# Performance work log

Measured on AMD Instinct MI355X. Metric: run time of the kernel, lower is better.

Reference implementation:

```python
import jax, jax.numpy as jnp
import numpy as np

EPS = 1e-8


def setup_inputs() -> dict:
    key = jax.random.key(0)
    ks = jax.random.split(key, 3)
    B, d_in, d_sae = 2048, 2048, 16384
    x = jax.random.normal(ks[0], (B, 2, d_in), dtype=jnp.float32)
    W_enc = jax.random.normal(ks[1], (d_in, d_sae), dtype=jnp.float32) / (d_in ** 0.5)
    W_dec = jax.random.normal(ks[2], (d_sae, d_in), dtype=jnp.float32) / (d_sae ** 0.5)
    b_enc = jnp.zeros((d_sae,), dtype=jnp.float32)
    b_dec = jnp.zeros((d_in,), dtype=jnp.float32)
    return {"x": x, "W_enc": W_enc, "W_dec": W_dec, "b_enc": b_enc,
            "b_dec": b_dec, "k": 64, "h": 8192}


def _encode(x, W_enc, b_enc, k):
    # x: (N, d_in) -> z: (N, d_sae), top-k sparsified with relu on kept values
    pre = x @ W_enc + b_enc
    v, i = jax.lax.top_k(pre, k)                       # (N, k)
    rows = jnp.arange(pre.shape[0])[:, None]
    return jnp.zeros_like(pre).at[rows, i].set(jax.nn.relu(v))


def _info_nce(z_a, z_b):
    z_a = z_a / jnp.maximum(jnp.linalg.norm(z_a, axis=-1, keepdims=True), EPS)
    z_b = z_b / jnp.maximum(jnp.linalg.norm(z_b, axis=-1, keepdims=True), EPS)
    sim = z_a @ z_b.T                                  # (B, B)
    diag = jnp.diagonal(sim)
    ce_row = jnp.mean(jax.nn.logsumexp(sim, axis=1) - diag)
    ce_col = jnp.mean(jax.nn.logsumexp(sim, axis=0) - diag)
    return 0.5 * (ce_row + ce_col)


def reference(x, W_enc, W_dec, b_enc, b_dec, k, h):
    alpha = 1.0
    B, _, d_in = x.shape
    # encode both tokens in one GEMM: (2B, d_in)
    x_flat = x.reshape(B * 2, d_in)
    z = _encode(x_flat, W_enc, b_enc, k)               # (2B, d_sae)
    x_hat_full = z @ W_dec + b_dec                     # (2B, d_in)
    x_hat_high = z[:, :h] @ W_dec[:h, :] + b_dec       # (2B, d_in)
    per_tok = d_in
    # mean over batch per token, summed over prev+cur (matches 4 separate means)
    se_full = jnp.sum((x_hat_full - x_flat) ** 2, axis=-1).reshape(B, 2)
    se_high = jnp.sum((x_hat_high - x_flat) ** 2, axis=-1).reshape(B, 2)
    l_matr = (jnp.mean(se_full, axis=0).sum() + jnp.mean(se_high, axis=0).sum()) / per_tok
    z2 = z.reshape(B, 2, -1)
    z_h_prev = z2[:, 0, :h]
    z_h_cur = z2[:, 1, :h]
    l_contr = _info_nce(z_h_cur, z_h_prev)
    total = l_matr + alpha * l_contr
    x_hat_cur = x_hat_full.reshape(B, 2, d_in)[:, 1]
    z_cur = z2[:, 1]
    return (total, x_hat_cur, z_cur)
```

## Files before the change

kernel.cpp:

```cpp
#include <hip/hip_runtime.h>
#include <hip/hip_bf16.h>
#include <math.h>

#define D_IN   2048
#define D_SAE  16384
#define NROWS  4096
#define KTOP   64
#define HDIM   8192
#define CHUNK  1024
#define EPSN   1e-8f
#define BANDW_F16 4e-3f
#define BANDW_F32 4e-4f
#define BANDCAP 512
#define NTILE   128
#define SEG     16
#define CAPT    (NTILE*SEG)
#define TH_CAND 2.0f

typedef unsigned short u16;
typedef unsigned char u8;
typedef _Float16 f16;
typedef __attribute__((ext_vector_type(8))) _Float16 f16x8;
typedef __attribute__((ext_vector_type(4))) _Float16 f16x4;
typedef __attribute__((ext_vector_type(8))) unsigned short u16x8;
typedef __attribute__((ext_vector_type(4))) float float4v;
typedef __attribute__((ext_vector_type(2))) float f32x2;

__device__ __forceinline__ unsigned f2u(float f) {
  unsigned b = __float_as_uint(f);
  return (b & 0x80000000u) ? ~b : (b | 0x80000000u);
}
__device__ __forceinline__ float u2f(unsigned u) {
  unsigned b = (u & 0x80000000u) ? (u & 0x7fffffffu) : ~u;
  return __uint_as_float(b);
}
__device__ __forceinline__ u16 f2bf_rne(float f) {
  unsigned b = __float_as_uint(f);
  unsigned r = (b + 0x7fffu + ((b >> 16) & 1u)) >> 16;
  return (u16)r;
}
__device__ __forceinline__ float bf2f(u16 u) {
  return __uint_as_float(((unsigned)u) << 16);
}
__device__ __forceinline__ void async_copy16(void* lds, const void* g) {
  __builtin_amdgcn_global_load_lds(
      (const __attribute__((address_space(1))) unsigned*)(g),
      (__attribute__((address_space(3))) unsigned*)(lds), 16, 0, 0);
}

__global__ __launch_bounds__(256)
void split_x_kernel(const float* __restrict__ x, f16* __restrict__ Axh)
{
  int t = blockIdx.x * blockDim.x + threadIdx.x;
  const int n4 = (NROWS * D_IN) / 4;
  if (t >= n4) return;
  float4 v = ((const float4*)x)[t];
  f16x4 h;
  h.x = (f16)v.x; h.y = (f16)v.y; h.z = (f16)v.z; h.w = (f16)v.w;
  ((f16x4*)Axh)[t] = h;
}

__global__ __launch_bounds__(256)
void splitT_w_kernel(const float* __restrict__ W,
                     f16* __restrict__ Th, float* __restrict__ WT)
{
  __shared__ float S[64][65];
  const int tx = threadIdx.x & 63, ty = threadIdx.x >> 6;
  const int n0 = blockIdx.x * 64, k0 = blockIdx.y * 64;
#pragma unroll
  for (int i = 0; i < 16; ++i) {
    int kl = ty + i * 4;
    S[kl][tx] = W[(size_t)(k0 + kl) * D_SAE + n0 + tx];
  }
  __syncthreads();
#pragma unroll
  for (int i = 0; i < 16; ++i) {
    int nl = ty + i * 4;
    float v = S[tx][nl];
    Th[(size_t)(n0 + nl) * D_IN + k0 + tx] = (f16)v;
    WT[(size_t)(n0 + nl) * D_IN + k0 + tx] = v;
  }
}

__global__ __launch_bounds__(256)
void wdec_to_fp8_kernel(const float* __restrict__ W,
                        u8* __restrict__ W8, float* __restrict__ scl)
{
  __shared__ float red[256];
  const int c = blockIdx.x;
  const int tid = threadIdx.x;
  const int e0 = tid * 8;
  const float* wr = W + (size_t)c * 2048;
  float4 a = *(const float4*)(wr + e0);
  float4 b = *(const float4*)(wr + e0 + 4);
  float w[8] = {a.x,a.y,a.z,a.w,b.x,b.y,b.z,b.w};
  float mx = 0.f;
#pragma unroll
  for (int i = 0; i < 8; ++i) mx = fmaxf(mx, fabsf(w[i]));
  red[tid] = mx; __syncthreads();
  for (int s = 128; s > 0; s >>= 1) { if (tid < s) red[tid] = fmaxf(red[tid], red[tid+s]); __syncthreads(); }
  const float mxa = red[0];
  const float senc = mxa > 0.f ? 448.f / mxa : 0.f;
  float q[8];
#pragma unroll
  for (int i = 0; i < 8; ++i) q[i] = fminf(fmaxf(w[i] * senc, -448.f), 448.f);
  int p0 = __builtin_amdgcn_cvt_pk_fp8_f32(q[0], q[1], 0, false);
  p0 = __builtin_amdgcn_cvt_pk_fp8_f32(q[2], q[3], p0, true);
  int p1 = __builtin_amdgcn_cvt_pk_fp8_f32(q[4], q[5], 0, false);
  p1 = __builtin_amdgcn_cvt_pk_fp8_f32(q[6], q[7], p1, true);
  uint2 o; o.x = (unsigned)p0; o.y = (unsigned)p1;
  *(uint2*)(W8 + (size_t)c * 2048 + e0) = o;
  if (tid == 0) scl[c] = mxa > 0.f ? mxa / 448.f : 0.f;
}

__global__ __launch_bounds__(256, 4)
void gemm_f16_kernel(const f16* __restrict__ Axh,
                     const f16* __restrict__ BT,
                     const float* __restrict__ bias,
                     unsigned* __restrict__ ckey_g,
                     u16* __restrict__ cidx_g,
                     unsigned* __restrict__ ccnt)
{
  __shared__ u16 sA[2][128 * 32];
  __shared__ u16 sB[2][128 * 32];
  const int tid = threadIdx.x;
  const int wave = tid >> 6, lane = tid & 63;
  const int bid = blockIdx.x;
  const int chunk = bid >> 10;
  const int b10 = bid & 1023;
  const int xcd = b10 & 7, loc = b10 >> 3;
  const int n0 = (xcd * 16 + (loc >> 3)) * 128;
  const int m0 = (loc & 7) * 128;
  const int row_base = chunk * CHUNK;
  const f16* A = Axh + (size_t)chunk * CHUNK * D_IN;
  const int wm = (wave >> 1) * 64, wn = (wave & 1) * 64;
  const int fr = lane & 15, fkg = lane >> 4;

  float4v acc[4][4];
#pragma unroll
  for (int i = 0; i < 4; ++i)
#pragma unroll
    for (int j = 0; j < 4; ++j) acc[i][j] = (float4v){0.f, 0.f, 0.f, 0.f};

  int aoff[4], boff[4];
#pragma unroll
  for (int mi = 0; mi < 4; ++mi) {
    int r = wm + mi * 16 + fr;
    aoff[mi] = r * 32 + ((fkg ^ ((r >> 1) & 3)) * 8);
    int c = wn + mi * 16 + fr;
    boff[mi] = c * 32 + ((fkg ^ ((c >> 1) & 3)) * 8);
  }

  auto stage = [&](int b, int k0) {
#pragma unroll
    for (int i = 0; i < 4; ++i) {
      int n = (i * 4 + wave) * 64 + lane;
      if (n < 512) {
        int row = n >> 2, s = n & 3;
        int fg = s ^ ((row >> 1) & 3);
        async_copy16((char*)&sA[b][0] + (size_t)n * 16,
                     A + (size_t)(m0 + row) * D_IN + k0 + fg * 8);
      } else {
        int n2 = n - 512;
        int row = n2 >> 2, s = n2 & 3;
        int fg = s ^ ((row >> 1) & 3);
        async_copy16((char*)&sB[b][0] + (size_t)n2 * 16,
                     BT + (size_t)(n0 + row) * D_IN + k0 + fg * 8);
      }
    }
  };

  stage(0, 0);
  __syncthreads();
  for (int t = 0; t < 64; ++t) {
    const int cur = t & 1;
    if (t < 63) stage(cur ^ 1, (t + 1) * 32);
    f16x8 a[4], b[4];
#pragma unroll
    for (int mi = 0; mi < 4; ++mi)
      a[mi] = *(const f16x8*)&sA[cur][aoff[mi]];
#pragma unroll
    for (int ni = 0; ni < 4; ++ni)
      b[ni] = *(const f16x8*)&sB[cur][boff[ni]];
#pragma unroll
    for (int mi = 0; mi < 4; ++mi)
#pragma unroll
      for (int ni = 0; ni < 4; ++ni)
        acc[mi][ni] = __builtin_amdgcn_mfma_f32_16x16x32_f16(a[mi], b[ni], acc[mi][ni], 0, 0, 0);
    __syncthreads();
  }

  unsigned* lcnt = (unsigned*)&sA[0][0];
  if (tid < 128) lcnt[tid] = 0u;
  __syncthreads();
  const int tileIdx = n0 >> 7;
  const int orow = (lane >> 4) * 4;
#pragma unroll
  for (int mi = 0; mi < 4; ++mi) {
#pragma unroll
    for (int ni = 0; ni < 4; ++ni) {
      int col = n0 + wn + ni * 16 + fr;
      float bv = bias[col];
#pragma unroll
      for (int rr = 0; rr < 4; ++rr) {
        float val = acc[mi][ni][rr] + bv;
        if (val >= TH_CAND) {
          int lrow = wm + mi * 16 + orow + rr;
          unsigned j = atomicAdd(&lcnt[lrow], 1u);
          if (j < SEG) {
            size_t sb = ((size_t)(row_base + m0 + lrow) * NTILE + tileIdx) * SEG;
            ckey_g[sb + j] = f2u(val);
            cidx_g[sb + j] = (u16)col;
          }
        }
      }
    }
  }
  __syncthreads();
  if (tid < 128)
    ccnt[(size_t)(row_base + m0 + tid) * NTILE + tileIdx] = lcnt[tid];
}

__global__ __launch_bounds__(256)
void select_compact_kernel(const unsigned* __restrict__ ckey_g,
                           const u16* __restrict__ cidx_g,
                           const unsigned* __restrict__ ccnt,
                           const float* __restrict__ x,
                           const float* __restrict__ WT,
                           const float* __restrict__ benc,
                           float bandw,
                           int*   __restrict__ topk_idx,
                           float* __restrict__ topk_val,
                           float* __restrict__ nh_norm,
                           unsigned* __restrict__ flags)
{
  __shared__ unsigned ckey[CAPT];
  __shared__ u16      cidx[CAPT];
  __shared__ unsigned tof[128];
  __shared__ unsigned tc[128];
  __shared__ unsigned hist[256];
  __shared__ unsigned sscan[257];
  __shared__ unsigned wsum[4];
  __shared__ float    bv_l[64];
  __shared__ int      band_idx[BANDCAP];
  __shared__ float    band_val[BANDCAP];
  __shared__ double   band_ex[BANDCAP];
  __shared__ unsigned char picked[BANDCAP];
  __shared__ int      out_idx[64];
  __shared__ float    out_val[64];
  __shared__ float    sh_v64;
  __shared__ unsigned sh_mcnt, sh_bstar, sh_kth, sh_ocnt, sh_bcnt, sh_bad;

  const int tid = threadIdx.x;
  const int wv = tid >> 6, ln = tid & 63;
  const int r = blockIdx.x;

  if (tid == 0) { sh_ocnt = 0u; sh_bcnt = 0u; sh_bad = 0u; sh_mcnt = 0u; sh_bstar = 0xffffffffu; }
  hist[tid] = 0u;
  if (tid < 128) {
    unsigned c = ccnt[(size_t)r * NTILE + tid];
    tc[tid] = c;
    if (c > SEG) sh_bad = 1u;
  }
  __syncthreads();
  if (tid < 128) {
    unsigned v = tc[tid];
#pragma unroll
    for (int d = 1; d < 64; d <<= 1) {
      unsigned t = __shfl_up(v, d);
      if (ln >= d) v += t;
    }
    tof[tid] = v;
  }
  __syncthreads();
  if (tid >= 64 && tid < 128) tof[tid] += tof[63];
  __syncthreads();
  const unsigned cc_u = tof[127];
  const int cc = (int)(cc_u < CAPT ? cc_u : CAPT);

  {
    unsigned ck[8]; u16 ci[8]; unsigned pv[8];
#pragma unroll
    for (int b = 0; b < 8; ++b) {
      int idx = tid + 256 * b;
      int tile = idx >> 4, slot = idx & 15;
      unsigned c = tc[tile]; if (c > SEG) c = SEG;
      bool valid = (unsigned)slot < c;
      pv[b] = valid ? (tof[tile] - tc[tile] + slot) : 0xffffffffu;
      ck[b] = valid ? ckey_g[(size_t)r * CAPT + idx] : 0u;
      ci[b] = valid ? cidx_g[(size_t)r * CAPT + idx] : (u16)0;
    }
#pragma unroll
    for (int b = 0; b < 8; ++b) {
      if (pv[b] < (unsigned)CAPT) { ckey[pv[b]] = ck[b]; cidx[pv[b]] = ci[b]; }
    }
  }
  __syncthreads();

  bool bad = (sh_bad != 0u) || (cc_u < 64u) || (cc_u > (unsigned)CAPT);

  if (!bad) {
    for (int s = tid; s < cc; s += 256) {
      float v = u2f(ckey[s]);
      int b = (int)((v - TH_CAND) * 100.0f);
      b = b < 0 ? 0 : (b > 255 ? 255 : b);
      atomicAdd(&hist[b], 1u);
    }
  }
  __syncthreads();
  {
    int rt = 255 - tid;
    unsigned v = hist[rt];
#pragma unroll
    for (int d = 1; d < 64; d <<= 1) {
      unsigned t = __shfl_up(v, d);
      if (ln >= d) v += t;
    }
    if (ln == 63) wsum[wv] = v;
    __syncthreads();
    unsigned add = 0;
    for (int w = 0; w < wv; ++w) add += wsum[w];
    sscan[rt] = v + add;
    if (tid == 0) sscan[256] = 0u;
    __syncthreads();
    if (sscan[tid] >= 64u && sscan[tid + 1] < 64u) {
      sh_bstar = (unsigned)tid;
      sh_kth = 64u - sscan[tid + 1];
    }
  }
  __syncthreads();

  if (bad || sh_bstar == 0xffffffffu) { if (tid == 0) flags[r] = 1u; return; }
  const int bstar = (int)sh_bstar;
  const unsigned kth = sh_kth;

  for (int s = tid; s < cc; s += 256) {
    float v = u2f(ckey[s]);
    int b = (int)((v - TH_CAND) * 100.0f);
    b = b < 0 ? 0 : (b > 255 ? 255 : b);
    if (b == bstar) {
      unsigned p = atomicAdd(&sh_mcnt, 1u);
      if (p < 64u) bv_l[p] = v;
    }
  }
  __syncthreads();
  if (sh_mcnt > 64u) { if (tid == 0) flags[r] = 1u; return; }
  const int m = (int)sh_mcnt;
  if (wv == 0 && ln < m) {
    float mine = bv_l[ln];
    int rank = 0;
    for (int j = 0; j < m; ++j) {
      float o = bv_l[j];
      if (o > mine || (o == mine && j < ln)) ++rank;
    }
    if (rank == (int)kth - 1) sh_v64 = mine;
  }
  __syncthreads();
  const float v64 = sh_v64;

  const float hi = v64 + 2.f * bandw, lo = v64 - 2.f * bandw;
  for (int s = tid; s < cc; s += 256) {
    float v = u2f(ckey[s]);
    int i = (int)cidx[s];
    if (v > hi) {
      unsigned p = atomicAdd(&sh_ocnt, 1u);
      out_idx[p] = i; out_val[p] = v;
    } else if (v >= lo) {
      unsigned p = atomicAdd(&sh_bcnt, 1u);
      if (p < BANDCAP) { band_idx[p] = i; band_val[p] = v; }
    }
  }
  __syncthreads();
  if (sh_bcnt > BANDCAP) { if (tid == 0) flags[r] = 1u; return; }
  const unsigned nci = sh_ocnt;
  const unsigned bcnt = sh_bcnt;
  const unsigned remaining = 64u - nci;

  if (bcnt == remaining) {
    for (unsigned s = tid; s < bcnt; s += 256) {
      out_idx[nci + s] = band_idx[s];
      out_val[nci + s] = band_val[s];
    }
    __syncthreads();
  } else {
    const float* xr = x + (size_t)r * 2048;
    for (unsigned bi = wv; bi < bcnt; bi += 4) {
      int c = band_idx[bi];
      const float* wr = WT + (size_t)c * 2048;
      double s = 0.0;
      for (int j0 = 0; j0 < 2048; j0 += 512) {
        float xa[8], wa[8];
#pragma unroll
        for (int u = 0; u < 8; ++u) {
          int j = j0 + ln + 64 * u;
          xa[u] = xr[j];
          wa[u] = wr[j];
        }
#pragma unroll
        for (int u = 0; u < 8; ++u)
          s += (double)xa[u] * (double)wa[u];
      }
#pragma unroll
      for (int off2 = 32; off2 > 0; off2 >>= 1)
        s += __shfl_down(s, off2);
      if (ln == 0) band_ex[bi] = s + (double)benc[c];
    }
    __syncthreads();
    if (tid == 0) {
      for (unsigned i2 = 0; i2 < bcnt; ++i2) picked[i2] = 0;
      for (unsigned s = 0; s < remaining; ++s) {
        int best = -1;
        for (unsigned b2 = 0; b2 < bcnt; ++b2) {
          if (picked[b2]) continue;
          if (best < 0 || band_ex[b2] > band_ex[best] ||
              (band_ex[b2] == band_ex[best] && band_idx[b2] < band_idx[best]))
            best = (int)b2;
        }
        picked[best] = 1;
        out_idx[nci + s] = band_idx[best];
        out_val[nci + s] = (float)band_ex[best];
      }
    }
    __syncthreads();
  }

  if (tid < 64) {
    float v = out_val[tid];
    v = v > 0.f ? v : 0.f;
    out_val[tid] = v;
    topk_idx[(size_t)r * 64 + tid] = out_idx[tid];
    topk_val[(size_t)r * 64 + tid] = v;
  }
  __syncthreads();
  if (tid == 0) {
    float n2 = 0.f;
    for (int s = 0; s < 64; ++s)
      if (out_idx[s] < HDIM) n2 += out_val[s] * out_val[s];
    nh_norm[r] = sqrtf(n2);
  }
}

__global__ __launch_bounds__(256)
void repair_kernel(const unsigned* __restrict__ flags,
                   const float* __restrict__ x,
                   const float* __restrict__ WT,
                   const float* __restrict__ benc,
                   int* __restrict__ topk_idx,
                   float* __restrict__ topk_val,
                   float* __restrict__ nh_norm)
{
  const int r = blockIdx.x;
  if (flags[r] == 0u) return;
  __shared__ float prerow[16384];
  __shared__ float xs[2048];
  __shared__ float rv[256];
  __shared__ int   ri[256];
  __shared__ int   oi[64];
  __shared__ float ov[64];
  const int tid = threadIdx.x;
  for (int i = tid; i < 2048; i += 256) xs[i] = x[(size_t)r * 2048 + i];
  __syncthreads();
  for (int c = tid; c < 16384; c += 256) {
    const float* wr = WT + (size_t)c * 2048;
    float s = 0.f;
    for (int j = 0; j < 2048; ++j) s = fmaf(xs[j], wr[j], s);
    prerow[c] = s + benc[c];
  }
  __syncthreads();
  for (int k2 = 0; k2 < 64; ++k2) {
    float bv = -INFINITY; int bi = 16384;
    for (int c = tid; c < 16384; c += 256) {
      float v = prerow[c];
      if (v > bv || (v == bv && c < bi)) { bv = v; bi = c; }
    }
    rv[tid] = bv; ri[tid] = bi;
    __syncthreads();
    for (int s2 = 128; s2 > 0; s2 >>= 1) {
      if (tid < s2) {
        if (rv[tid+s2] > rv[tid] || (rv[tid+s2] == rv[tid] && ri[tid+s2] < ri[tid])) {
          rv[tid] = rv[tid+s2]; ri[tid] = ri[tid+s2];
        }
      }
      __syncthreads();
    }
    if (tid == 0) { oi[k2] = ri[0]; ov[k2] = rv[0]; prerow[ri[0]] = -INFINITY; }
    __syncthreads();
  }
  if (tid < 64) {
    float v = ov[tid]; v = v > 0.f ? v : 0.f;
    topk_idx[(size_t)r * 64 + tid] = oi[tid];
    topk_val[(size_t)r * 64 + tid] = v;
  }
  __syncthreads();
  if (tid == 0) {
    float n2 = 0.f;
    for (int s = 0; s < 64; ++s)
      if (oi[s] < HDIM) { float v = ov[s] > 0.f ? ov[s] : 0.f; n2 += v * v; }
    nh_norm[r] = sqrtf(n2);
  }
}

__global__ __launch_bounds__(256)
void gemm_pre_kernel(const float* __restrict__ A,
                     const float* __restrict__ B,
                     const float* __restrict__ bias,
                     float* __restrict__ C)
{
  __shared__ float As[16][129];
  __shared__ float Bs[16][129];
  const int tid = threadIdx.x;
  const int tx = tid & 15, ty = tid >> 4;
  const int m0 = blockIdx.y * 128;
  const int n0 = blockIdx.x * 128;
  float acc[8][8];
#pragma unroll
  for (int i = 0; i < 8; ++i)
#pragma unroll
    for (int j = 0; j < 8; ++j) acc[i][j] = 0.f;
  const int lk = tid & 15, lm = tid >> 4;
  for (int k0 = 0; k0 < 2048; k0 += 16) {
#pragma unroll
    for (int i = 0; i < 8; ++i) {
      int m = lm + 16 * i;
      As[lk][m] = A[(size_t)(m0 + m) * 2048 + k0 + lk];
    }
#pragma unroll
    for (int i = 0; i < 8; ++i) {
      int idx = tid + 256 * i;
      int kk = idx >> 7, nn = idx & 127;
      Bs[kk][nn] = B[(size_t)(k0 + kk) * 16384 + n0 + nn];
    }
    __syncthreads();
#pragma unroll
    for (int kk = 0; kk < 16; ++kk) {
      float a[8], b[8];
#pragma unroll
      for (int i = 0; i < 8; ++i) a[i] = As[kk][ty + 16 * i];
#pragma unroll
      for (int j = 0; j < 8; ++j) b[j] = Bs[kk][tx + 16 * j];
#pragma unroll
      for (int i = 0; i < 8; ++i)
#pragma unroll
        for (int j = 0; j < 8; ++j) acc[i][j] = fmaf(a[i], b[j], acc[i][j]);
    }
    __syncthreads();
  }
#pragma unroll
  for (int i = 0; i < 8; ++i) {
    int m = m0 + ty + 16 * i;
#pragma unroll
    for (int j = 0; j < 8; ++j) {
      int n = n0 + tx + 16 * j;
      C[(size_t)m * 16384 + n] = acc[i][j] + bias[n];
    }
  }
}

__global__ __launch_bounds__(256)
void select_fb_kernel(const float* __restrict__ pre,
                      const float* __restrict__ x,
                      const float* __restrict__ Wenc,
                      const float* __restrict__ benc,
                      int row_base, float bandw,
                      int*   __restrict__ topk_idx,
                      float* __restrict__ topk_val,
                      float* __restrict__ nh_norm)
{
  __shared__ unsigned hist[256];
  __shared__ int      band_idx[BANDCAP];
  __shared__ double   band_ex[BANDCAP];
  __shared__ double   red_d[256];
  __shared__ int      out_idx[64];
  __shared__ float    out_val[64];
  __shared__ unsigned char picked[BANDCAP];
  __shared__ unsigned sh_prefix, sh_need, sh_ocnt, sh_bcnt;

  const int tid = threadIdx.x;
  const int lrow = blockIdx.x;
  const int row = row_base + lrow;
  const float* prow = pre + (size_t)lrow * 16384;

  if (tid == 0) { sh_prefix = 0u; sh_need = 64u; }
  __syncthreads();
  for (int level = 24; level >= 0; level -= 8) {
    hist[tid] = 0u;
    __syncthreads();
    unsigned prefix = sh_prefix;
    for (int i = tid; i < 16384; i += 256) {
      unsigned u = f2u(prow[i]);
      bool match = (level == 24) || ((u >> ((level + 8) & 31)) == prefix);
      if (match) atomicAdd(&hist[(u >> level) & 255u], 1u);
    }
    __syncthreads();
    if (tid == 0) {
      unsigned need = sh_need, acc = 0; int q = 0;
      for (int b2 = 255; b2 >= 0; --b2) {
        if (acc + hist[b2] >= need) { q = b2; break; }
        acc += hist[b2];
      }
      sh_prefix = (prefix << 8) | (unsigned)q;
      sh_need = need - acc;
    }
    __syncthreads();
  }
  const float v64 = u2f(sh_prefix);

  if (tid == 0) { sh_ocnt = 0u; sh_bcnt = 0u; }
  __syncthreads();
  const float hi = v64 + 2.f * bandw, lo = v64 - 2.f * bandw;
  for (int i = tid; i < 16384; i += 256) {
    float v = prow[i];
    if (v > hi) {
      unsigned p = atomicAdd(&sh_ocnt, 1u);
      out_idx[p] = i; out_val[p] = v;
    } else if (v >= lo) {
      unsigned p = atomicAdd(&sh_bcnt, 1u);
      if (p < BANDCAP) { band_idx[p] = i; }
    }
  }
  __syncthreads();
  const unsigned nci = sh_ocnt;
  const unsigned bcnt = sh_bcnt < BANDCAP ? sh_bcnt : BANDCAP;
  const unsigned remaining = 64u - nci;

  if (bcnt == remaining) {
    for (unsigned s = tid; s < bcnt; s += 256) {
      int c = band_idx[s];
      out_idx[nci + s] = c;
      out_val[nci + s] = prow[c];
    }
    __syncthreads();
  } else {
    const float* xr = x + (size_t)row * 2048;
    for (unsigned bi = 0; bi < bcnt; ++bi) {
      int c = band_idx[bi];
      double part = 0.0;
#pragma unroll
      for (int j2 = 0; j2 < 8; ++j2) {
        int kk = tid + 256 * j2;
        part += (double)xr[kk] * (double)Wenc[(size_t)kk * 16384 + c];
      }
      red_d[tid] = part;
      __syncthreads();
      for (int sft = 128; sft > 0; sft >>= 1) {
        if (tid < sft) red_d[tid] += red_d[tid + sft];
        __syncthreads();
      }
      if (tid == 0) band_ex[bi] = red_d[0] + (double)benc[c];
      __syncthreads();
    }
    if (tid == 0) {
      for (unsigned i2 = 0; i2 < bcnt; ++i2) picked[i2] = 0;
      for (unsigned s = 0; s < remaining; ++s) {
        int best = -1;
        for (unsigned b2 = 0; b2 < bcnt; ++b2) {
          if (picked[b2]) continue;
          if (best < 0 || band_ex[b2] > band_ex[best] ||
              (band_ex[b2] == band_ex[best] && band_idx[b2] < band_idx[best]))
            best = (int)b2;
        }
        picked[best] = 1;
        out_idx[nci + s] = band_idx[best];
        out_val[nci + s] = (float)band_ex[best];
      }
    }
    __syncthreads();
  }

  if (tid < 64) {
    float v = out_val[tid];
    v = v > 0.f ? v : 0.f;
    out_val[tid] = v;
    topk_idx[(size_t)row * 64 + tid] = out_idx[tid];
    topk_val[(size_t)row * 64 + tid] = v;
  }
  __syncthreads();
  if (tid == 0) {
    float n2 = 0.f;
    for (int s = 0; s < 64; ++s)
      if (out_idx[s] < HDIM) n2 += out_val[s] * out_val[s];
    nh_norm[row] = sqrtf(n2);
  }
}

__global__ __launch_bounds__(256)
void scatter_kernel(const int* __restrict__ topk_idx,
                    const float* __restrict__ topk_val,
                    const float* __restrict__ nh_norm,
                    float* __restrict__ zcur_out,
                    u16* __restrict__ ZpTb)
{
  int t = blockIdx.x * blockDim.x + threadIdx.x;
  if (t >= NROWS * 64) return;
  int r = t >> 6;
  int c = topk_idx[t];
  float v = topk_val[t];
  int b = r >> 1;
  if (r & 1) {
    zcur_out[(size_t)b * 16384 + c] = v;
  } else if (c < HDIM) {
    float nrm = nh_norm[r]; nrm = nrm > EPSN ? nrm : EPSN;
    ZpTb[(size_t)c * 2048 + b] = f2bf_rne(v / nrm);
  }
}

__global__ __launch_bounds__(256)
void scatter_f32_kernel(const int* __restrict__ topk_idx,
                        const float* __restrict__ topk_val,
                        const float* __restrict__ nh_norm,
                        float* __restrict__ zcur_out,
                        float* __restrict__ ZpT)
{
  int t = blockIdx.x * blockDim.x + threadIdx.x;
  if (t >= NROWS * 64) return;
  int r = t >> 6;
  int c = topk_idx[t];
  float v = topk_val[t];
  int b = r >> 1;
  if (r & 1) {
    zcur_out[(size_t)b * 16384 + c] = v;
  } else if (c < HDIM) {
    float nrm = nh_norm[r]; nrm = nrm > EPSN ? nrm : EPSN;
    ZpT[(size_t)c * 2048 + b] = v / nrm;
  }
}

__global__ __launch_bounds__(256)
void decode_kernel(const int* __restrict__ topk_idx,
                   const float* __restrict__ topk_val,
                   const u8* __restrict__ W8,
                   const float* __restrict__ scl,
                   const float* __restrict__ bdec,
                   const float* __restrict__ x,
                   float* __restrict__ se_full,
                   float* __restrict__ se_high,
                   float* __restrict__ xhat_out)
{
  __shared__ int sidx[64];
  __shared__ float sval[64];
  __shared__ float red[256];
  const int tid = threadIdx.x;
  const int r = blockIdx.x;
  const int e0 = tid * 8;
  if (tid < 64) {
    int c = topk_idx[(size_t)r*64+tid];
    sidx[tid] = c;
    sval[tid] = topk_val[(size_t)r*64+tid] * scl[c];
  }
  __syncthreads();
  float accf[8], acch[8];
  {
    float4 b0 = *(const float4*)(bdec + e0);
    float4 b1 = *(const float4*)(bdec + e0 + 4);
    accf[0]=b0.x; accf[1]=b0.y; accf[2]=b0.z; accf[3]=b0.w;
    accf[4]=b1.x; accf[5]=b1.y; accf[6]=b1.z; accf[7]=b1.w;
#pragma unroll
    for (int i = 0; i < 8; ++i) acch[i] = accf[i];
  }
  for (int s0 = 0; s0 < 64; s0 += 8) {
    uint2 w[8]; float vf[8], vh[8];
#pragma unroll
    for (int j = 0; j < 8; ++j) {
      int c = sidx[s0 + j];
      float v = sval[s0 + j];
      vf[j] = v;
      vh[j] = (c < HDIM) ? v : 0.f;
      w[j] = *(const uint2*)(W8 + (size_t)c * 2048 + e0);
    }
#pragma unroll
    for (int j = 0; j < 8; ++j) {
      f32x2 f0 = __builtin_amdgcn_cvt_pk_f32_fp8((int)w[j].x, false);
      f32x2 f1 = __builtin_amdgcn_cvt_pk_f32_fp8((int)w[j].x, true);
      f32x2 f2 = __builtin_amdgcn_cvt_pk_f32_fp8((int)w[j].y, false);
      f32x2 f3 = __builtin_amdgcn_cvt_pk_f32_fp8((int)w[j].y, true);
      float wvv[8] = {f0[0],f0[1],f1[0],f1[1],f2[0],f2[1],f3[0],f3[1]};
#pragma unroll
      for (int i = 0; i < 8; ++i) {
        accf[i] = fmaf(vf[j], wvv[i], accf[i]);
        acch[i] = fmaf(vh[j], wvv[i], acch[i]);
      }
    }
  }
  const float* xr = x + (size_t)r * 2048;
  float4 x0 = *(const float4*)(xr + e0);
  float4 x1 = *(const float4*)(xr + e0 + 4);
  float xv[8] = {x0.x,x0.y,x0.z,x0.w,x1.x,x1.y,x1.z,x1.w};
  float sf = 0.f, shs = 0.f;
#pragma unroll
  for (int i = 0; i < 8; ++i) {
    float df = accf[i] - xv[i]; sf += df*df;
    float dh = acch[i] - xv[i]; shs += dh*dh;
  }
  red[tid] = sf; __syncthreads();
  for (int s2=128; s2>0; s2>>=1){ if (tid<s2) red[tid]+=red[tid+s2]; __syncthreads(); }
  if (tid==0) se_full[r] = red[0];
  __syncthreads();
  red[tid] = shs; __syncthreads();
  for (int s2=128; s2>0; s2>>=1){ if (tid<s2) red[tid]+=red[tid+s2]; __syncthreads(); }
  if (tid==0) se_high[r] = red[0];
  if (r & 1) {
    float* orow = xhat_out + (size_t)(r >> 1) * 2048;
    float4 o0 = {accf[0],accf[1],accf[2],accf[3]};
    float4 o1 = {accf[4],accf[5],accf[6],accf[7]};
    *(float4*)(orow + e0) = o0;
    *(float4*)(orow + e0 + 4) = o1;
  }
}

__global__ __launch_bounds__(256)
void decode_f32_kernel(const int* __restrict__ topk_idx,
                       const float* __restrict__ topk_val,
                       const float* __restrict__ Wdec,
                       const float* __restrict__ bdec,
                       const float* __restrict__ x,
                       float* __restrict__ se_full,
                       float* __restrict__ se_high,
                       float* __restrict__ xhat_out)
{
  __shared__ int sidx[64];
  __shared__ float sval[64];
  __shared__ float red[256];
  const int tid = threadIdx.x;
  const int r = blockIdx.x;
  if (tid < 64) { sidx[tid] = topk_idx[(size_t)r*64+tid]; sval[tid] = topk_val[(size_t)r*64+tid]; }
  __syncthreads();
  float accf[8], acch[8];
#pragma unroll
  for (int i = 0; i < 8; ++i) { float b = bdec[tid + 256*i]; accf[i] = b; acch[i] = b; }
  for (int s = 0; s < 64; ++s) {
    int c = sidx[s]; float v = sval[s];
    const float* wr = Wdec + (size_t)c * 2048;
    bool high = (c < HDIM);
#pragma unroll
    for (int i = 0; i < 8; ++i) {
      float w = wr[tid + 256*i];
      accf[i] = fmaf(v, w, accf[i]);
      if (high) acch[i] = fmaf(v, w, acch[i]);
    }
  }
  const float* xr = x + (size_t)r * 2048;
  float sf = 0.f, shs = 0.f;
#pragma unroll
  for (int i = 0; i < 8; ++i) {
    float xv = xr[tid + 256*i];
    float df = accf[i] - xv; sf += df*df;
    float dh = acch[i] - xv; shs += dh*dh;
  }
  red[tid] = sf; __syncthreads();
  for (int s2=128; s2>0; s2>>=1){ if (tid<s2) red[tid]+=red[tid+s2]; __syncthreads(); }
  if (tid==0) se_full[r] = red[0];
  __syncthreads();
  red[tid] = shs; __syncthreads();
  for (int s2=128; s2>0; s2>>=1){ if (tid<s2) red[tid]+=red[tid+s2]; __syncthreads(); }
  if (tid==0) se_high[r] = red[0];
  if (r & 1) {
    float* orow = xhat_out + (size_t)(r >> 1) * 2048;
#pragma unroll
    for (int i = 0; i < 8; ++i) orow[tid + 256*i] = accf[i];
  }
}

__global__ __launch_bounds__(256)
void sim_kernel(const int* __restrict__ topk_idx,
                const float* __restrict__ topk_val,
                const float* __restrict__ nh_norm,
                const u16* __restrict__ ZpTb,
                float* __restrict__ sim)
{
  __shared__ int cidx2[64];
  __shared__ float cval2[64];
  __shared__ int scnt;
  const int tid = threadIdx.x;
  const int i = blockIdx.x;
  const int r = 2 * i + 1;
  const int e0 = tid * 8;
  if (tid == 0) scnt = 0;
  __syncthreads();
  if (tid < 64) {
    int c = topk_idx[(size_t)r*64+tid];
    float v = topk_val[(size_t)r*64+tid];
    if (c < HDIM) {
      float nrm = nh_norm[r]; nrm = nrm > EPSN ? nrm : EPSN;
      int p = atomicAdd(&scnt, 1);
      cidx2[p] = c; cval2[p] = v / nrm;
    }
  }
  __syncthreads();
  float acc[8];
#pragma unroll
  for (int ii = 0; ii < 8; ++ii) acc[ii] = 0.f;
  const int m = scnt;
  int s = 0;
  for (; s + 8 <= m; s += 8) {
    u16x8 z[8]; float vv[8];
#pragma unroll
    for (int j = 0; j < 8; ++j) {
      vv[j] = cval2[s + j];
      z[j] = *(const u16x8*)(ZpTb + (size_t)cidx2[s + j] * 2048 + e0);
    }
#pragma unroll
    for (int j = 0; j < 8; ++j)
#pragma unroll
      for (int ii = 0; ii < 8; ++ii)
        acc[ii] = fmaf(vv[j], bf2f(z[j][ii]), acc[ii]);
  }
  for (; s < m; ++s) {
    int c = cidx2[s]; float v = cval2[s];
    u16x8 z8 = *(const u16x8*)(ZpTb + (size_t)c * 2048 + e0);
#pragma unroll
    for (int ii = 0; ii < 8; ++ii)
      acc[ii] = fmaf(v, bf2f(z8[ii]), acc[ii]);
  }
  float* srow = sim + (size_t)i * 2048;
  float4 o0 = {acc[0],acc[1],acc[2],acc[3]};
  float4 o1 = {acc[4],acc[5],acc[6],acc[7]};
  *(float4*)(srow + e0) = o0;
  *(float4*)(srow + e0 + 4) = o1;
}

__global__ __launch_bounds__(256)
void sim_f32_kernel(const int* __restrict__ topk_idx,
                    const float* __restrict__ topk_val,
                    const float* __restrict__ nh_norm,
                    const float* __restrict__ ZpT,
                    float* __restrict__ sim)
{
  __shared__ int cidx2[64];
  __shared__ float cval2[64];
  __shared__ int scnt;
  const int tid = threadIdx.x;
  const int i = blockIdx.x;
  const int r = 2 * i + 1;
  if (tid == 0) scnt = 0;
  __syncthreads();
  if (tid < 64) {
    int c = topk_idx[(size_t)r*64+tid];
    float v = topk_val[(size_t)r*64+tid];
    if (c < HDIM) {
      float nrm = nh_norm[r]; nrm = nrm > EPSN ? nrm : EPSN;
      int p = atomicAdd(&scnt, 1);
      cidx2[p] = c; cval2[p] = v / nrm;
    }
  }
  __syncthreads();
  float acc[8];
#pragma unroll
  for (int ii = 0; ii < 8; ++ii) acc[ii] = 0.f;
  int m = scnt;
  for (int s = 0; s < m; ++s) {
    int c = cidx2[s]; float v = cval2[s];
    const float* zr = ZpT + (size_t)c * 2048;
#pragma unroll
    for (int ii = 0; ii < 8; ++ii)
      acc[ii] = fmaf(v, zr[tid + 256*ii], acc[ii]);
  }
  float* srow = sim + (size_t)i * 2048;
#pragma unroll
  for (int ii = 0; ii < 8; ++ii) srow[tid + 256*ii] = acc[ii];
}

__global__ __launch_bounds__(256)
void lse_row_kernel(const float* __restrict__ sim,
                    float* __restrict__ lse_row, float* __restrict__ diag)
{
  __shared__ float red[256];
  const int tid = threadIdx.x; const int i = blockIdx.x;
  const int e0 = tid * 8;
  const float* srow = sim + (size_t)i * 2048;
  float4 v0 = *(const float4*)(srow + e0);
  float4 v1 = *(const float4*)(srow + e0 + 4);
  float vals[8] = {v0.x,v0.y,v0.z,v0.w,v1.x,v1.y,v1.z,v1.w};
  float mx = -INFINITY;
#pragma unroll
  for (int ii=0; ii<8; ++ii) mx = fmaxf(mx, vals[ii]);
  if ((i >> 3) == tid) diag[i] = vals[i & 7];
  red[tid]=mx; __syncthreads();
  for (int s=128;s>0;s>>=1){ if (tid<s) red[tid]=fmaxf(red[tid],red[tid+s]); __syncthreads(); }
  mx = red[0]; __syncthreads();
  float se=0.f;
#pragma unroll
  for (int ii=0;ii<8;++ii) se += expf(vals[ii]-mx);
  red[tid]=se; __syncthreads();
  for (int s=128;s>0;s>>=1){ if (tid<s) red[tid]+=red[tid+s]; __syncthreads(); }
  if (tid==0) lse_row[i] = mx + logf(red[0]);
}

__global__ __launch_bounds__(256)
void lse_col_kernel(const float* __restrict__ sim, float* __restrict__ lse_col)
{
  __shared__ float ml[32][9], sl[32][9];
  const int tid = threadIdx.x;
  const int c = tid & 7, rr = tid >> 3;
  const int col = blockIdx.x * 8 + c;
  float m = -INFINITY, s = 0.f;
  for (int r = rr; r < 2048; r += 32) {
    float v = sim[(size_t)r * 2048 + col];
    float mn = fmaxf(m, v);
    s = s * expf(m - mn) + expf(v - mn);
    m = mn;
  }
  ml[rr][c] = m; sl[rr][c] = s;
  __syncthreads();
  if (rr == 0) {
    float M = ml[0][c];
#pragma unroll
    for (int i = 1; i < 32; ++i) M = fmaxf(M, ml[i][c]);
    float S = 0.f;
#pragma unroll
    for (int i = 0; i < 32; ++i) S += sl[i][c] * expf(ml[i][c] - M);
    lse_col[col] = M + logf(S);
  }
}

__global__ __launch_bounds__(256)
void final_kernel(const float* __restrict__ se_full, const float* __restrict__ se_high,
                  const float* __restrict__ lse_row, const float* __restrict__ lse_col,
                  const float* __restrict__ diag, float* __restrict__ out0)
{
  __shared__ float red[256];
  const int tid = threadIdx.x;
  float s1 = 0.f;
  for (int i = tid; i < 4096; i += 256) s1 += se_full[i] + se_high[i];
  red[tid]=s1; __syncthreads();
  for (int s=128;s>0;s>>=1){ if (tid<s) red[tid]+=red[tid+s]; __syncthreads(); }
  float matr = red[0]; __syncthreads();
  float s2 = 0.f;
  for (int i = tid; i < 2048; i += 256) s2 += (lse_row[i]-diag[i]) + (lse_col[i]-diag[i]);
  red[tid]=s2; __syncthreads();
  for (int s=128;s>0;s>>=1){ if (tid<s) red[tid]+=red[tid+s]; __syncthreads(); }
  if (tid == 0) {
    float l_matr  = matr / (2048.f * 2048.f);
    float l_contr = 0.5f * (red[0] / 2048.f);
    out0[0] = l_matr + l_contr;
  }
}

extern "C" void kernel_launch(void* const* d_in, const int* in_sizes, int n_in,
                              void* d_out, int out_size, void* d_ws, size_t ws_size,
                              hipStream_t stream)
{
  const float* x    = (const float*)d_in[0];
  const float* Wenc = (const float*)d_in[1];
  const float* Wdec = (const float*)d_in[2];
  const float* benc = (const float*)d_in[3];
  const float* bdec = (const float*)d_in[4];
  float* out = (float*)d_out;
  float* xhat_out = out + 1;
  float* zcur_out = out + 1 + (size_t)2048 * 2048;
  (void)in_sizes; (void)n_in; (void)out_size;

  char* ws = (char*)d_ws;
  size_t off = 0;
  auto alloc = [&](size_t bytes) {
    char* p = ws + off; off += (bytes + 255) & ~(size_t)255; return p;
  };
  int*      tki     = (int*)     alloc((size_t)NROWS * 64 * 4);
  float*    tkv     = (float*)   alloc((size_t)NROWS * 64 * 4);
  float*    nh_norm = (float*)   alloc((size_t)NROWS * 4);
  float*    se_f    = (float*)   alloc((size_t)NROWS * 4);
  float*    se_h    = (float*)   alloc((size_t)NROWS * 4);
  float*    lse_r   = (float*)   alloc((size_t)2048 * 4);
  float*    lse_c   = (float*)   alloc((size_t)2048 * 4);
  float*    diag    = (float*)   alloc((size_t)2048 * 4);
  f16*      Axh     = (f16*)     alloc((size_t)NROWS * D_IN * 2);
  unsigned* ckey_g  = (unsigned*)alloc((size_t)NROWS * CAPT * 4);
  u16*      cidx_g  = (u16*)     alloc((size_t)NROWS * CAPT * 2);
  unsigned* ccnt    = (unsigned*)alloc((size_t)NROWS * NTILE * 4);
  unsigned* flags   = (unsigned*)alloc((size_t)NROWS * 4);
  char*     R1      = alloc((size_t)D_SAE * D_IN * 2);
  char*     R2      = alloc((size_t)D_SAE * D_IN * 4);
  size_t need = off;

  f16*   Th    = (f16*)R1;
  u8*    W8    = (u8*)R1;
  float* scl   = (float*)(R1 + (size_t)D_SAE * D_IN);
  float* WT    = (float*)R2;
  u16*   ZpTb  = (u16*)R2;
  float* simb  = (float*)(R2 + (size_t)8192 * 2048 * 2);

  hipMemsetAsync(zcur_out, 0, (size_t)2048 * 16384 * 4, stream);

  if (ws_size >= need) {
    split_x_kernel<<<(NROWS * D_IN / 4 + 255) / 256, 256, 0, stream>>>(x, Axh);
    {
      dim3 g(D_SAE / 64, D_IN / 64);
      splitT_w_kernel<<<g, 256, 0, stream>>>(Wenc, Th, WT);
    }
    hipMemsetAsync(flags, 0, (size_t)NROWS * 4, stream);
    gemm_f16_kernel<<<4096, 256, 0, stream>>>(Axh, Th, benc, ckey_g, cidx_g, ccnt);
    select_compact_kernel<<<NROWS, 256, 0, stream>>>(ckey_g, cidx_g, ccnt, x, WT, benc,
        BANDW_F16, tki, tkv, nh_norm, flags);
    repair_kernel<<<NROWS, 256, 0, stream>>>(flags, x, WT, benc, tki, tkv, nh_norm);
    wdec_to_fp8_kernel<<<D_SAE, 256, 0, stream>>>(Wdec, W8, scl);
    hipMemsetAsync(ZpTb, 0, (size_t)8192 * 2048 * 2, stream);
    scatter_kernel<<<(NROWS * 64) / 256, 256, 0, stream>>>(tki, tkv, nh_norm, zcur_out, ZpTb);
    decode_kernel<<<NROWS, 256, 0, stream>>>(tki, tkv, W8, scl, bdec, x, se_f, se_h, xhat_out);
    sim_kernel<<<2048, 256, 0, stream>>>(tki, tkv, nh_norm, ZpTb, simb);
    lse_row_kernel<<<2048, 256, 0, stream>>>(simb, lse_r, diag);
    lse_col_kernel<<<256, 256, 0, stream>>>(simb, lse_c);
    final_kernel<<<1, 256, 0, stream>>>(se_f, se_h, lse_r, lse_c, diag, out);
  } else {
    off = 0;
    float* pre2  = (float*)alloc((size_t)CHUNK * 16384 * 4);
    int*   tki2  = (int*)  alloc((size_t)NROWS * 64 * 4);
    float* tkv2  = (float*)alloc((size_t)NROWS * 64 * 4);
    float* nh2   = (float*)alloc((size_t)NROWS * 4);
    float* sef2  = (float*)alloc((size_t)NROWS * 4);
    float* seh2  = (float*)alloc((size_t)NROWS * 4);
    float* lr2   = (float*)alloc((size_t)2048 * 4);
    float* lc2   = (float*)alloc((size_t)2048 * 4);
    float* dg2   = (float*)alloc((size_t)2048 * 4);
    float* ZpT2  = (float*)alloc((size_t)8192 * 2048 * 4);
    float* sim2  = (float*)alloc((size_t)2048 * 2048 * 4);
    for (int ch = 0; ch < 4; ++ch) {
      dim3 g(128, 8);
      gemm_pre_kernel<<<g, 256, 0, stream>>>(x + (size_t)ch * CHUNK * 2048, Wenc, benc, pre2);
      select_fb_kernel<<<CHUNK, 256, 0, stream>>>(pre2, x, Wenc, benc,
          ch * CHUNK, BANDW_F32, tki2, tkv2, nh2);
    }
    hipMemsetAsync(ZpT2, 0, (size_t)8192 * 2048 * 4, stream);
    scatter_f32_kernel<<<(NROWS * 64) / 256, 256, 0, stream>>>(tki2, tkv2, nh2, zcur_out, ZpT2);
    decode_f32_kernel<<<NROWS, 256, 0, stream>>>(tki2, tkv2, Wdec, bdec, x, sef2, seh2, xhat_out);
    sim_f32_kernel<<<2048, 256, 0, stream>>>(tki2, tkv2, nh2, ZpT2, sim2);
    lse_row_kernel<<<2048, 256, 0, stream>>>(sim2, lr2, dg2);
    lse_col_kernel<<<256, 256, 0, stream>>>(sim2, lc2);
    final_kernel<<<1, 256, 0, stream>>>(sef2, seh2, lr2, lc2, dg2, out);
  }
}
```

Before: 715.5 us.

## Fuse prep kernels and merge decode, similarity and row-LSE into one token kernel

```diff
diff --git a/kernel.cpp b/kernel.cpp
--- a/kernel.cpp
+++ b/kernel.cpp
@@ -49,36 +49,37 @@
 }
 
 __global__ __launch_bounds__(256)
-void split_x_kernel(const float* __restrict__ x, f16* __restrict__ Axh)
-{
-  int t = blockIdx.x * blockDim.x + threadIdx.x;
-  const int n4 = (NROWS * D_IN) / 4;
-  if (t >= n4) return;
-  float4 v = ((const float4*)x)[t];
-  f16x4 h;
-  h.x = (f16)v.x; h.y = (f16)v.y; h.z = (f16)v.z; h.w = (f16)v.w;
-  ((f16x4*)Axh)[t] = h;
-}
-
-__global__ __launch_bounds__(256)
-void splitT_w_kernel(const float* __restrict__ W,
-                     f16* __restrict__ Th, float* __restrict__ WT)
+void pre_kernel(const float* __restrict__ x, const float* __restrict__ W,
+                f16* __restrict__ Axh, f16* __restrict__ Th,
+                float* __restrict__ WT)
 {
   __shared__ float S[64][65];
-  const int tx = threadIdx.x & 63, ty = threadIdx.x >> 6;
-  const int n0 = blockIdx.x * 64, k0 = blockIdx.y * 64;
-#pragma unroll
-  for (int i = 0; i < 16; ++i) {
-    int kl = ty + i * 4;
-    S[kl][tx] = W[(size_t)(k0 + kl) * D_SAE + n0 + tx];
-  }
-  __syncthreads();
-#pragma unroll
-  for (int i = 0; i < 16; ++i) {
-    int nl = ty + i * 4;
-    float v = S[tx][nl];
-    Th[(size_t)(n0 + nl) * D_IN + k0 + tx] = (f16)v;
-    WT[(size_t)(n0 + nl) * D_IN + k0 + tx] = v;
+  const int bid = blockIdx.x;
+  if (bid < 8192) {
+    const int tx = threadIdx.x & 63, ty = threadIdx.x >> 6;
+    const int n0 = (bid & 255) * 64, k0 = (bid >> 8) * 64;
+#pragma unroll
+    for (int i = 0; i < 16; ++i) {
+      int kl = ty + i * 4;
+      S[kl][tx] = W[(size_t)(k0 + kl) * D_SAE + n0 + tx];
+    }
+    __syncthreads();
+#pragma unroll
+    for (int i = 0; i < 16; ++i) {
+      int nl = ty + i * 4;
+      float v = S[tx][nl];
+      Th[(size_t)(n0 + nl) * D_IN + k0 + tx] = (f16)v;
+      WT[(size_t)(n0 + nl) * D_IN + k0 + tx] = v;
+    }
+  } else {
+    int t = (bid - 8192) * 256 + threadIdx.x;
+    const int n4 = (NROWS * D_IN) / 4;
+    if (t < n4) {
+      float4 v = ((const float4*)x)[t];
+      f16x4 h;
+      h.x = (f16)v.x; h.y = (f16)v.y; h.z = (f16)v.z; h.w = (f16)v.w;
+      ((f16x4*)Axh)[t] = h;
+    }
   }
 }
 
@@ -437,6 +438,7 @@
     for (int s = 0; s < 64; ++s)
       if (out_idx[s] < HDIM) n2 += out_val[s] * out_val[s];
     nh_norm[r] = sqrtf(n2);
+    flags[r] = 0u;
   }
 }
 
@@ -498,6 +500,177 @@
       if (oi[s] < HDIM) { float v = ov[s] > 0.f ? ov[s] : 0.f; n2 += v * v; }
     nh_norm[r] = sqrtf(n2);
   }
+}
+
+__global__ __launch_bounds__(256)
+void scatter_kernel(const int* __restrict__ topk_idx,
+                    const float* __restrict__ topk_val,
+                    const float* __restrict__ nh_norm,
+                    float* __restrict__ zcur_out,
+                    u16* __restrict__ ZpTb)
+{
+  int t = blockIdx.x * blockDim.x + threadIdx.x;
+  if (t >= NROWS * 64) return;
+  int r = t >> 6;
+  int c = topk_idx[t];
+  float v = topk_val[t];
+  int b = r >> 1;
+  if (r & 1) {
+    zcur_out[(size_t)b * 16384 + c] = v;
+  } else if (c < HDIM) {
+    float nrm = nh_norm[r]; nrm = nrm > EPSN ? nrm : EPSN;
+    ZpTb[(size_t)c * 2048 + b] = f2bf_rne(v / nrm);
+  }
+}
+
+__global__ __launch_bounds__(256)
+void token_kernel(const int* __restrict__ topk_idx,
+                  const float* __restrict__ topk_val,
+                  const u8* __restrict__ W8,
+                  const float* __restrict__ scl,
+                  const float* __restrict__ bdec,
+                  const float* __restrict__ x,
+                  const float* __restrict__ nh_norm,
+                  const u16* __restrict__ ZpTb,
+                  float* __restrict__ se_full,
+                  float* __restrict__ se_high,
+                  float* __restrict__ xhat_out,
+                  float* __restrict__ simb,
+                  float* __restrict__ lse_row,
+                  float* __restrict__ diag)
+{
+  __shared__ int sidx[64];
+  __shared__ float sval[64];
+  __shared__ float red[256];
+  __shared__ int cidx2[64];
+  __shared__ float cval2[64];
+  __shared__ int scnt;
+  const int tid = threadIdx.x;
+  const int r = blockIdx.x;
+  const int e0 = tid * 8;
+  if (tid == 0) scnt = 0;
+  if (tid < 64) {
+    int c = topk_idx[(size_t)r*64+tid];
+    sidx[tid] = c;
+    sval[tid] = topk_val[(size_t)r*64+tid] * scl[c];
+  }
+  __syncthreads();
+  float accf[8], acch[8];
+  {
+    float4 b0 = *(const float4*)(bdec + e0);
+    float4 b1 = *(const float4*)(bdec + e0 + 4);
+    accf[0]=b0.x; accf[1]=b0.y; accf[2]=b0.z; accf[3]=b0.w;
+    accf[4]=b1.x; accf[5]=b1.y; accf[6]=b1.z; accf[7]=b1.w;
+#pragma unroll
+    for (int i = 0; i < 8; ++i) acch[i] = accf[i];
+  }
+  for (int s0 = 0; s0 < 64; s0 += 8) {
+    uint2 w[8]; float vf[8], vh[8];
+#pragma unroll
+    for (int j = 0; j < 8; ++j) {
+      int c = sidx[s0 + j];
+      float v = sval[s0 + j];
+      vf[j] = v;
+      vh[j] = (c < HDIM) ? v : 0.f;
+      w[j] = *(const uint2*)(W8 + (size_t)c * 2048 + e0);
+    }
+#pragma unroll
+    for (int j = 0; j < 8; ++j) {
+      f32x2 f0 = __builtin_amdgcn_cvt_pk_f32_fp8((int)w[j].x, false);
+      f32x2 f1 = __builtin_amdgcn_cvt_pk_f32_fp8((int)w[j].x, true);
+      f32x2 f2 = __builtin_amdgcn_cvt_pk_f32_fp8((int)w[j].y, false);
+      f32x2 f3 = __builtin_amdgcn_cvt_pk_f32_fp8((int)w[j].y, true);
+      float wvv[8] = {f0[0],f0[1],f1[0],f1[1],f2[0],f2[1],f3[0],f3[1]};
+#pragma unroll
+      for (int i = 0; i < 8; ++i) {
+        accf[i] = fmaf(vf[j], wvv[i], accf[i]);
+        acch[i] = fmaf(vh[j], wvv[i], acch[i]);
+      }
+    }
+  }
+  const float* xr = x + (size_t)r * 2048;
+  float4 x0 = *(const float4*)(xr + e0);
+  float4 x1 = *(const float4*)(xr + e0 + 4);
+  float xv[8] = {x0.x,x0.y,x0.z,x0.w,x1.x,x1.y,x1.z,x1.w};
+  float sf = 0.f, shs = 0.f;
+#pragma unroll
+  for (int i = 0; i < 8; ++i) {
+    float df = accf[i] - xv[i]; sf += df*df;
+    float dh = acch[i] - xv[i]; shs += dh*dh;
+  }
+  red[tid] = sf; __syncthreads();
+  for (int s2=128; s2>0; s2>>=1){ if (tid<s2) red[tid]+=red[tid+s2]; __syncthreads(); }
+  if (tid==0) se_full[r] = red[0];
+  __syncthreads();
+  red[tid] = shs; __syncthreads();
+  for (int s2=128; s2>0; s2>>=1){ if (tid<s2) red[tid]+=red[tid+s2]; __syncthreads(); }
+  if (tid==0) se_high[r] = red[0];
+  if (!(r & 1)) return;
+
+  {
+    float* orow = xhat_out + (size_t)(r >> 1) * 2048;
+    float4 o0 = {accf[0],accf[1],accf[2],accf[3]};
+    float4 o1 = {accf[4],accf[5],accf[6],accf[7]};
+    *(float4*)(orow + e0) = o0;
+    *(float4*)(orow + e0 + 4) = o1;
+  }
+  const int i = r >> 1;
+  __syncthreads();
+  if (tid < 64) {
+    int c = sidx[tid];
+    float v = topk_val[(size_t)r*64+tid];
+    if (c < HDIM) {
+      float nrm = nh_norm[r]; nrm = nrm > EPSN ? nrm : EPSN;
+      int p = atomicAdd(&scnt, 1);
+      cidx2[p] = c; cval2[p] = v / nrm;
+    }
+  }
+  __syncthreads();
+  float acc[8];
+#pragma unroll
+  for (int ii = 0; ii < 8; ++ii) acc[ii] = 0.f;
+  const int m = scnt;
+  int s = 0;
+  for (; s + 8 <= m; s += 8) {
+    u16x8 z[8]; float vv[8];
+#pragma unroll
+    for (int j = 0; j < 8; ++j) {
+      vv[j] = cval2[s + j];
+      z[j] = *(const u16x8*)(ZpTb + (size_t)cidx2[s + j] * 2048 + e0);
+    }
+#pragma unroll
+    for (int j = 0; j < 8; ++j)
+#pragma unroll
+      for (int ii = 0; ii < 8; ++ii)
+        acc[ii] = fmaf(vv[j], bf2f(z[j][ii]), acc[ii]);
+  }
+  for (; s < m; ++s) {
+    int c = cidx2[s]; float v = cval2[s];
+    u16x8 z8 = *(const u16x8*)(ZpTb + (size_t)c * 2048 + e0);
+#pragma unroll
+    for (int ii = 0; ii < 8; ++ii)
+      acc[ii] = fmaf(v, bf2f(z8[ii]), acc[ii]);
+  }
+  {
+    float* srow = simb + (size_t)i * 2048;
+    float4 o0 = {acc[0],acc[1],acc[2],acc[3]};
+    float4 o1 = {acc[4],acc[5],acc[6],acc[7]};
+    *(float4*)(srow + e0) = o0;
+    *(float4*)(srow + e0 + 4) = o1;
+  }
+  float mx = -INFINITY;
+#pragma unroll
+  for (int ii = 0; ii < 8; ++ii) mx = fmaxf(mx, acc[ii]);
+  if ((i >> 3) == tid) diag[i] = acc[i & 7];
+  red[tid] = mx; __syncthreads();
+  for (int s2=128; s2>0; s2>>=1){ if (tid<s2) red[tid]=fmaxf(red[tid],red[tid+s2]); __syncthreads(); }
+  mx = red[0]; __syncthreads();
+  float se = 0.f;
+#pragma unroll
+  for (int ii = 0; ii < 8; ++ii) se += expf(acc[ii] - mx);
+  red[tid] = se; __syncthreads();
+  for (int s2=128; s2>0; s2>>=1){ if (tid<s2) red[tid]+=red[tid+s2]; __syncthreads(); }
+  if (tid == 0) lse_row[i] = mx + logf(red[0]);
 }
 
 __global__ __launch_bounds__(256)
@@ -684,27 +857,6 @@
 }
 
 __global__ __launch_bounds__(256)
-void scatter_kernel(const int* __restrict__ topk_idx,
-                    const float* __restrict__ topk_val,
-                    const float* __restrict__ nh_norm,
-                    float* __restrict__ zcur_out,
-                    u16* __restrict__ ZpTb)
-{
-  int t = blockIdx.x * blockDim.x + threadIdx.x;
-  if (t >= NROWS * 64) return;
-  int r = t >> 6;
-  int c = topk_idx[t];
-  float v = topk_val[t];
-  int b = r >> 1;
-  if (r & 1) {
-    zcur_out[(size_t)b * 16384 + c] = v;
-  } else if (c < HDIM) {
-    float nrm = nh_norm[r]; nrm = nrm > EPSN ? nrm : EPSN;
-    ZpTb[(size_t)c * 2048 + b] = f2bf_rne(v / nrm);
-  }
-}
-
-__global__ __launch_bounds__(256)
 void scatter_f32_kernel(const int* __restrict__ topk_idx,
                         const float* __restrict__ topk_val,
                         const float* __restrict__ nh_norm,
@@ -726,88 +878,6 @@
 }
 
 __global__ __launch_bounds__(256)
-void decode_kernel(const int* __restrict__ topk_idx,
-                   const float* __restrict__ topk_val,
-                   const u8* __restrict__ W8,
-                   const float* __restrict__ scl,
-                   const float* __restrict__ bdec,
-                   const float* __restrict__ x,
-                   float* __restrict__ se_full,
-                   float* __restrict__ se_high,
-                   float* __restrict__ xhat_out)
-{
-  __shared__ int sidx[64];
-  __shared__ float sval[64];
-  __shared__ float red[256];
-  const int tid = threadIdx.x;
-  const int r = blockIdx.x;
-  const int e0 = tid * 8;
-  if (tid < 64) {
-    int c = topk_idx[(size_t)r*64+tid];
-    sidx[tid] = c;
-    sval[tid] = topk_val[(size_t)r*64+tid] * scl[c];
-  }
-  __syncthreads();
-  float accf[8], acch[8];
-  {
-    float4 b0 = *(const float4*)(bdec + e0);
-    float4 b1 = *(const float4*)(bdec + e0 + 4);
-    accf[0]=b0.x; accf[1]=b0.y; accf[2]=b0.z; accf[3]=b0.w;
-    accf[4]=b1.x; accf[5]=b1.y; accf[6]=b1.z; accf[7]=b1.w;
-#pragma unroll
-    for (int i = 0; i < 8; ++i) acch[i] = accf[i];
-  }
-  for (int s0 = 0; s0 < 64; s0 += 8) {
-    uint2 w[8]; float vf[8], vh[8];
-#pragma unroll
-    for (int j = 0; j < 8; ++j) {
-      int c = sidx[s0 + j];
-      float v = sval[s0 + j];
-      vf[j] = v;
-      vh[j] = (c < HDIM) ? v : 0.f;
-      w[j] = *(const uint2*)(W8 + (size_t)c * 2048 + e0);
-    }
-#pragma unroll
-    for (int j = 0; j < 8; ++j) {
-      f32x2 f0 = __builtin_amdgcn_cvt_pk_f32_fp8((int)w[j].x, false);
-      f32x2 f1 = __builtin_amdgcn_cvt_pk_f32_fp8((int)w[j].x, true);
-      f32x2 f2 = __builtin_amdgcn_cvt_pk_f32_fp8((int)w[j].y, false);
-      f32x2 f3 = __builtin_amdgcn_cvt_pk_f32_fp8((int)w[j].y, true);
-      float wvv[8] = {f0[0],f0[1],f1[0],f1[1],f2[0],f2[1],f3[0],f3[1]};
-#pragma unroll
-      for (int i = 0; i < 8; ++i) {
-        accf[i] = fmaf(vf[j], wvv[i], accf[i]);
-        acch[i] = fmaf(vh[j], wvv[i], acch[i]);
-      }
-    }
-  }
-  const float* xr = x + (size_t)r * 2048;
-  float4 x0 = *(const float4*)(xr + e0);
-  float4 x1 = *(const float4*)(xr + e0 + 4);
-  float xv[8] = {x0.x,x0.y,x0.z,x0.w,x1.x,x1.y,x1.z,x1.w};
-  float sf = 0.f, shs = 0.f;
-#pragma unroll
-  for (int i = 0; i < 8; ++i) {
-    float df = accf[i] - xv[i]; sf += df*df;
-    float dh = acch[i] - xv[i]; shs += dh*dh;
-  }
-  red[tid] = sf; __syncthreads();
-  for (int s2=128; s2>0; s2>>=1){ if (tid<s2) red[tid]+=red[tid+s2]; __syncthreads(); }
-  if (tid==0) se_full[r] = red[0];
-  __syncthreads();
-  red[tid] = shs; __syncthreads();
-  for (int s2=128; s2>0; s2>>=1){ if (tid<s2) red[tid]+=red[tid+s2]; __syncthreads(); }
-  if (tid==0) se_high[r] = red[0];
-  if (r & 1) {
-    float* orow = xhat_out + (size_t)(r >> 1) * 2048;
-    float4 o0 = {accf[0],accf[1],accf[2],accf[3]};
-    float4 o1 = {accf[4],accf[5],accf[6],accf[7]};
-    *(float4*)(orow + e0) = o0;
-    *(float4*)(orow + e0 + 4) = o1;
-  }
-}
-
-__global__ __launch_bounds__(256)
 void decode_f32_kernel(const int* __restrict__ topk_idx,
                        const float* __restrict__ topk_val,
                        const float* __restrict__ Wdec,
@@ -858,64 +928,6 @@
 #pragma unroll
     for (int i = 0; i < 8; ++i) orow[tid + 256*i] = accf[i];
   }
-}
-
-__global__ __launch_bounds__(256)
-void sim_kernel(const int* __restrict__ topk_idx,
-                const float* __restrict__ topk_val,
-                const float* __restrict__ nh_norm,
-                const u16* __restrict__ ZpTb,
-                float* __restrict__ sim)
-{
-  __shared__ int cidx2[64];
-  __shared__ float cval2[64];
-  __shared__ int scnt;
-  const int tid = threadIdx.x;
-  const int i = blockIdx.x;
-  const int r = 2 * i + 1;
-  const int e0 = tid * 8;
-  if (tid == 0) scnt = 0;
-  __syncthreads();
-  if (tid < 64) {
-    int c = topk_idx[(size_t)r*64+tid];
-    float v = topk_val[(size_t)r*64+tid];
-    if (c < HDIM) {
-      float nrm = nh_norm[r]; nrm = nrm > EPSN ? nrm : EPSN;
-      int p = atomicAdd(&scnt, 1);
-      cidx2[p] = c; cval2[p] = v / nrm;
-    }
-  }
-  __syncthreads();
-  float acc[8];
-#pragma unroll
-  for (int ii = 0; ii < 8; ++ii) acc[ii] = 0.f;
-  const int m = scnt;
-  int s = 0;
-  for (; s + 8 <= m; s += 8) {
-    u16x8 z[8]; float vv[8];
-#pragma unroll
-    for (int j = 0; j < 8; ++j) {
-      vv[j] = cval2[s + j];
-      z[j] = *(const u16x8*)(ZpTb + (size_t)cidx2[s + j] * 2048 + e0);
-    }
-#pragma unroll
-    for (int j = 0; j < 8; ++j)
-#pragma unroll
-      for (int ii = 0; ii < 8; ++ii)
-        acc[ii] = fmaf(vv[j], bf2f(z[j][ii]), acc[ii]);
-  }
-  for (; s < m; ++s) {
-    int c = cidx2[s]; float v = cval2[s];
-    u16x8 z8 = *(const u16x8*)(ZpTb + (size_t)c * 2048 + e0);
-#pragma unroll
-    for (int ii = 0; ii < 8; ++ii)
-      acc[ii] = fmaf(v, bf2f(z8[ii]), acc[ii]);
-  }
-  float* srow = sim + (size_t)i * 2048;
-  float4 o0 = {acc[0],acc[1],acc[2],acc[3]};
-  float4 o1 = {acc[4],acc[5],acc[6],acc[7]};
-  *(float4*)(srow + e0) = o0;
-  *(float4*)(srow + e0 + 4) = o1;
 }
 
 __global__ __launch_bounds__(256)
@@ -1081,12 +1093,7 @@
   hipMemsetAsync(zcur_out, 0, (size_t)2048 * 16384 * 4, stream);
 
   if (ws_size >= need) {
-    split_x_kernel<<<(NROWS * D_IN / 4 + 255) / 256, 256, 0, stream>>>(x, Axh);
-    {
-      dim3 g(D_SAE / 64, D_IN / 64);
-      splitT_w_kernel<<<g, 256, 0, stream>>>(Wenc, Th, WT);
-    }
-    hipMemsetAsync(flags, 0, (size_t)NROWS * 4, stream);
+    pre_kernel<<<16384, 256, 0, stream>>>(x, Wenc, Axh, Th, WT);
     gemm_f16_kernel<<<4096, 256, 0, stream>>>(Axh, Th, benc, ckey_g, cidx_g, ccnt);
     select_compact_kernel<<<NROWS, 256, 0, stream>>>(ckey_g, cidx_g, ccnt, x, WT, benc,
         BANDW_F16, tki, tkv, nh_norm, flags);
@@ -1094,9 +1101,8 @@
     wdec_to_fp8_kernel<<<D_SAE, 256, 0, stream>>>(Wdec, W8, scl);
     hipMemsetAsync(ZpTb, 0, (size_t)8192 * 2048 * 2, stream);
     scatter_kernel<<<(NROWS * 64) / 256, 256, 0, stream>>>(tki, tkv, nh_norm, zcur_out, ZpTb);
-    decode_kernel<<<NROWS, 256, 0, stream>>>(tki, tkv, W8, scl, bdec, x, se_f, se_h, xhat_out);
-    sim_kernel<<<2048, 256, 0, stream>>>(tki, tkv, nh_norm, ZpTb, simb);
-    lse_row_kernel<<<2048, 256, 0, stream>>>(simb, lse_r, diag);
+    token_kernel<<<NROWS, 256, 0, stream>>>(tki, tkv, W8, scl, bdec, x, nh_norm, ZpTb,
+        se_f, se_h, xhat_out, simb, lse_r, diag);
     lse_col_kernel<<<256, 256, 0, stream>>>(simb, lse_c);
     final_kernel<<<1, 256, 0, stream>>>(se_f, se_h, lse_r, lse_c, diag, out);
   } else {
```

New measurement: 719.5 us. No clear change (+0.6%).
